# Performance work log

Hardware: AMD Instinct MI355X
Metric: run time of the kernel (lower is better)

Reference implementation:

```python
import jax, jax.numpy as jnp
import numpy as np

EPS = 1e-12
NUM_ITERATIONS = 3


def squash(t, axis=-1):
    sn = jnp.sum(t * t, axis=axis, keepdims=True)
    scale = sn / (1.0 + sn + EPS)
    return scale * t / jnp.sqrt(sn + EPS)


def setup_inputs() -> dict:
    key = jax.random.key(0)
    k1, k2 = jax.random.split(key)
    B, R, IN, OUT, C = 128, 4096, 16, 32, 2
    x = jax.random.normal(k1, (B, R, IN), dtype=jnp.float32)
    # learned parameter: torch.randn(num_capsules, num_route_nodes, in, out)
    route_weights = jax.random.normal(k2, (C, R, IN, OUT), dtype=jnp.float32)
    return {"x": x, "route_weights": route_weights}


def reference(x, route_weights):
    # priors: [C, B, R, 1, O] == x[None,:,:,None,:] @ W[:,None,:,:,:]
    priors = jnp.einsum('bri,crio->cbro', x, route_weights)[..., None, :]
    # logits kept [C,B,R,1,1]: the torch code stores [C,B,R,1,O] but every
    # update (delta_logits) is constant along O, so softmax over axis=2 is identical.
    logits = jnp.zeros(priors.shape[:-1] + (1,), dtype=priors.dtype)
    outputs = None
    for i in range(NUM_ITERATIONS):
        probs = jax.nn.softmax(logits, axis=2)                      # over route nodes
        s = jnp.sum(probs * priors, axis=2, keepdims=True)          # [C,B,1,1,O]
        outputs = squash(s, axis=-1)
        if i != NUM_ITERATIONS - 1:
            delta = jnp.sum(priors * outputs, axis=-1, keepdims=True)  # [C,B,R,1,1]
            logits = logits + delta
    return outputs
```

## Files before the change

### kernel.cpp

```cpp
#include <hip/hip_runtime.h>
#include <math.h>

#define CB    128
#define CR    4096
#define CIN   16
#define COUT  32
#define CCAP  2
#define RC    16
#define NRCH  (CR / RC)
#define EPSF  1e-12f

typedef _Float16 h8  __attribute__((ext_vector_type(8)));
typedef _Float16 h4t __attribute__((ext_vector_type(4)));
typedef float    f4  __attribute__((ext_vector_type(4)));

__global__ __launch_bounds__(256) void caps_init_kernel(float* __restrict__ vsum)
{
  vsum[blockIdx.x * 256 + threadIdx.x] = 0.f;
}

__global__ __launch_bounds__(256) void caps_prepack_kernel(
    const float* __restrict__ w, _Float16* __restrict__ wp)
{
  const int blk = (int)blockIdx.x;
  const int c   = blk >> 10;
  const int r0  = (blk & 1023) * 4;
  const int t   = (int)threadIdx.x;

  __shared__ __align__(16) float Wl[4 * 512];
  {
    const float4* src = (const float4*)(w + ((size_t)c * CR + r0) * 512);
    ((float4*)Wl)[t]       = src[t];
    ((float4*)Wl)[t + 256] = src[t + 256];
  }
  __syncthreads();

#pragma unroll
  for (int s = 0; s < 2; ++s) {
    const int idx = t + s * 256;
    const int rr  = idx >> 7;
    const int rem = idx & 127;
    const int ot  = rem >> 6;
    const int L   = rem & 63;
    const int g   = L >> 4, m = L & 15;
    h4t v;
#pragma unroll
    for (int j = 0; j < 4; ++j)
      v[j] = (_Float16)Wl[rr * 512 + (4 * g + j) * 32 + ot * 16 + m];
    *(h4t*)(wp + ((((size_t)(c * CR + r0 + rr)) * 2 + ot) * 64 + L) * 4) = v;
  }
}

__global__ __launch_bounds__(512) void caps_pass_kernel(
    const float* __restrict__ x, const _Float16* __restrict__ wp,
    const float* __restrict__ vsum,
    float* __restrict__ partialA, float* __restrict__ partialE)
{
  const int blk = (int)blockIdx.x;
  const int c   = blk >> 8;
  const int rch = blk & 255;
  const int r0  = rch * RC;
  const int t   = (int)threadIdx.x;
  const int wv  = t >> 6;
  const int L   = t & 63;
  const int g   = L >> 4;
  const int m   = L & 15;
  const int b   = wv * 16 + m;

  __shared__ __align__(16) _Float16 WpL[RC * 512];
  __shared__ float OutL[128][40];

  {
    const int4* src = (const int4*)(wp + (size_t)(c * CR + r0) * 512);
    ((int4*)WpL)[t]       = src[t];
    ((int4*)WpL)[t + 512] = src[t + 512];
  }

  const float* vb = vsum + ((size_t)c * CB + b) * COUT;
  float4 vA = *(const float4*)(vb + 4 * g);
  float4 vB = *(const float4*)(vb + 16 + 4 * g);

  float accA[4] = {0.f, 0.f, 0.f, 0.f};
  float accB[4] = {0.f, 0.f, 0.f, 0.f};
  float esum = 0.f;

  __syncthreads();

#pragma unroll 4
  for (int ri = 0; ri < RC; ++ri) {
    const int r = r0 + ri;
    float4 xf = *(const float4*)(x + ((size_t)b * CR + r) * CIN + 4 * g);
    h8 bx = {(_Float16)xf.x, (_Float16)xf.y, (_Float16)xf.z, (_Float16)xf.w,
             (_Float16)0.f, (_Float16)0.f, (_Float16)0.f, (_Float16)0.f};
    h4t wA4 = *(const h4t*)(WpL + ri * 512 + L * 4);
    h4t wB4 = *(const h4t*)(WpL + ri * 512 + 256 + L * 4);
    h8 aA = {wA4[0], wA4[1], wA4[2], wA4[3],
             (_Float16)0.f, (_Float16)0.f, (_Float16)0.f, (_Float16)0.f};
    h8 aB = {wB4[0], wB4[1], wB4[2], wB4[3],
             (_Float16)0.f, (_Float16)0.f, (_Float16)0.f, (_Float16)0.f};
    f4 z = {0.f, 0.f, 0.f, 0.f};
    f4 pA = __builtin_amdgcn_mfma_f32_16x16x32_f16(aA, bx, z, 0, 0, 0);
    f4 pB = __builtin_amdgcn_mfma_f32_16x16x32_f16(aB, bx, z, 0, 0, 0);

    float d = pA[0] * vA.x + pA[1] * vA.y + pA[2] * vA.z + pA[3] * vA.w
            + pB[0] * vB.x + pB[1] * vB.y + pB[2] * vB.z + pB[3] * vB.w;
    d += __shfl_xor(d, 16);
    d += __shfl_xor(d, 32);

    const float e = __expf(d);
    esum += e;
#pragma unroll
    for (int j = 0; j < 4; ++j) { accA[j] += e * pA[j]; accB[j] += e * pB[j]; }
  }

#pragma unroll
  for (int j = 0; j < 4; ++j) {
    OutL[b][4 * g + j]      = accA[j];
    OutL[b][16 + 4 * g + j] = accB[j];
  }
  if (g == 0) OutL[b][32] = esum;
  __syncthreads();

  {
    const int bb = t >> 2, q = t & 3;
    float4 v0 = *(const float4*)&OutL[bb][q * 8];
    float4 v1 = *(const float4*)&OutL[bb][q * 8 + 4];
    float* dst = partialA + (((size_t)(c * NRCH + rch)) * CB + bb) * COUT + q * 8;
    *(float4*)dst = v0;
    *(float4*)(dst + 4) = v1;
    if (t < 128) partialE[((size_t)(c * NRCH + rch)) * CB + t] = OutL[t][32];
  }
}

__global__ __launch_bounds__(256) void caps_redv_kernel(
    const float* __restrict__ partialA, const float* __restrict__ partialE,
    float* __restrict__ vsum, float* __restrict__ out, int final_)
{
  const int cb = (int)blockIdx.x;
  const int c  = cb >> 7, b = cb & 127;
  const int t  = (int)threadIdx.x;
  const int o  = t & 31, jg = t >> 5;

  __shared__ float red[8][33];
  __shared__ float rede[8];

  float s = 0.f;
#pragma unroll 4
  for (int k = 0; k < 32; ++k) {
    const int j = jg + k * 8;
    s += partialA[(((size_t)(c * NRCH + j)) * CB + b) * COUT + o];
  }
  red[jg][o] = s;
  __syncthreads();

  if (t < 8) {
    float e = 0.f;
#pragma unroll 4
    for (int k = 0; k < 32; ++k)
      e += partialE[((size_t)(c * NRCH + t + k * 8)) * CB + b];
    rede[t] = e;
  }
  __syncthreads();

  if (t < 32) {
    float sv = red[0][t] + red[1][t] + red[2][t] + red[3][t] +
               red[4][t] + red[5][t] + red[6][t] + red[7][t];
    float es = rede[0] + rede[1] + rede[2] + rede[3] +
               rede[4] + rede[5] + rede[6] + rede[7];
    float sm = sv / es;
    float sn = sm * sm;
#pragma unroll
    for (int sh = 1; sh < 32; sh <<= 1) sn += __shfl_xor(sn, sh);
    float fac = sn / ((1.f + sn + EPSF) * sqrtf(sn + EPSF));
    float vv = sm * fac;
    if (final_) out[cb * COUT + t] = vv;
    else        vsum[cb * COUT + t] += vv;
  }
}

extern "C" void kernel_launch(void* const* d_in, const int* in_sizes, int n_in,
                              void* d_out, int out_size, void* d_ws, size_t ws_size,
                              hipStream_t stream) {
  const float* x = (const float*)d_in[0];
  const float* w = (const float*)d_in[1];
  float* out = (float*)d_out;

  char* p = (char*)d_ws;
  _Float16* wp = (_Float16*)p;
  p += (size_t)CCAP * CR * 512 * sizeof(_Float16);
  float* vsum = (float*)p;
  p += (size_t)CCAP * CB * COUT * sizeof(float);
  float* partialA = (float*)p;
  p += (size_t)CCAP * NRCH * CB * COUT * sizeof(float);
  float* partialE = (float*)p;

  caps_prepack_kernel<<<dim3(CCAP * 1024), 256, 0, stream>>>(w, wp);
  caps_init_kernel<<<dim3(32), 256, 0, stream>>>(vsum);
  for (int it = 0; it < 3; ++it) {
    caps_pass_kernel<<<dim3(CCAP * NRCH), 512, 0, stream>>>(x, wp, vsum, partialA, partialE);
    caps_redv_kernel<<<dim3(CCAP * CB), 256, 0, stream>>>(partialA, partialE, vsum, out,
                                                          it == 2 ? 1 : 0);
  }
}
```

Baseline: 75.45 us.

## Fuse weight fp16 packing into pass kernel and drop init/prepack launches

Removes the separate prepack kernel and the vsum zero-init kernel. Each pass block now loads fp32 route weights into LDS, repacks them to fp16 in the MFMA layout in registers, and writes them back into shared memory, reusing the same LDS buffer. The first iteration takes a uniform-logit path that skips the dot product, shuffles and exp, and redv writes vsum instead of accumulating. The cost is reading fp32 weights (twice the bytes) and converting them in all three passes, instead of reading a precomputed fp16 copy.

```diff
diff --git a/kernel.cpp b/kernel.cpp
--- a/kernel.cpp
+++ b/kernel.cpp
@@ -14,47 +14,11 @@
 typedef _Float16 h4t __attribute__((ext_vector_type(4)));
 typedef float    f4  __attribute__((ext_vector_type(4)));
 
-__global__ __launch_bounds__(256) void caps_init_kernel(float* __restrict__ vsum)
-{
-  vsum[blockIdx.x * 256 + threadIdx.x] = 0.f;
-}
-
-__global__ __launch_bounds__(256) void caps_prepack_kernel(
-    const float* __restrict__ w, _Float16* __restrict__ wp)
-{
-  const int blk = (int)blockIdx.x;
-  const int c   = blk >> 10;
-  const int r0  = (blk & 1023) * 4;
-  const int t   = (int)threadIdx.x;
-
-  __shared__ __align__(16) float Wl[4 * 512];
-  {
-    const float4* src = (const float4*)(w + ((size_t)c * CR + r0) * 512);
-    ((float4*)Wl)[t]       = src[t];
-    ((float4*)Wl)[t + 256] = src[t + 256];
-  }
-  __syncthreads();
-
-#pragma unroll
-  for (int s = 0; s < 2; ++s) {
-    const int idx = t + s * 256;
-    const int rr  = idx >> 7;
-    const int rem = idx & 127;
-    const int ot  = rem >> 6;
-    const int L   = rem & 63;
-    const int g   = L >> 4, m = L & 15;
-    h4t v;
-#pragma unroll
-    for (int j = 0; j < 4; ++j)
-      v[j] = (_Float16)Wl[rr * 512 + (4 * g + j) * 32 + ot * 16 + m];
-    *(h4t*)(wp + ((((size_t)(c * CR + r0 + rr)) * 2 + ot) * 64 + L) * 4) = v;
-  }
-}
-
 __global__ __launch_bounds__(512) void caps_pass_kernel(
-    const float* __restrict__ x, const _Float16* __restrict__ wp,
+    const float* __restrict__ x, const float* __restrict__ w,
     const float* __restrict__ vsum,
-    float* __restrict__ partialA, float* __restrict__ partialE)
+    float* __restrict__ partialA, float* __restrict__ partialE,
+    int uniform)
 {
   const int blk = (int)blockIdx.x;
   const int c   = blk >> 8;
@@ -67,18 +31,41 @@
   const int m   = L & 15;
   const int b   = wv * 16 + m;
 
-  __shared__ __align__(16) _Float16 WpL[RC * 512];
-  __shared__ float OutL[128][40];
+  __shared__ __align__(16) char lds[36864];
+  float*    Wst = (float*)lds;
+  _Float16* WpL = (_Float16*)lds;
+  float (*OutL)[40] = (float (*)[40])(lds + 16384);
 
   {
-    const int4* src = (const int4*)(wp + (size_t)(c * CR + r0) * 512);
-    ((int4*)WpL)[t]       = src[t];
-    ((int4*)WpL)[t + 512] = src[t + 512];
+    const float4* src = (const float4*)(w + ((size_t)c * CR + r0) * 512);
+#pragma unroll
+    for (int k = 0; k < 4; ++k) ((float4*)Wst)[t + k * 512] = src[t + k * 512];
   }
+  __syncthreads();
 
-  const float* vb = vsum + ((size_t)c * CB + b) * COUT;
-  float4 vA = *(const float4*)(vb + 4 * g);
-  float4 vB = *(const float4*)(vb + 16 + 4 * g);
+  h4t pk[4];
+#pragma unroll
+  for (int q = 0; q < 4; ++q) {
+    const int sl  = t * 4 + q;
+    const int rr  = sl >> 7;
+    const int rem = sl & 127;
+    const int ot  = rem >> 6;
+    const int Ls  = rem & 63;
+    const int gs  = Ls >> 4, ms = Ls & 15;
+#pragma unroll
+    for (int j = 0; j < 4; ++j)
+      pk[q][j] = (_Float16)Wst[rr * 512 + (4 * gs + j) * 32 + ot * 16 + ms];
+  }
+  __syncthreads();
+#pragma unroll
+  for (int q = 0; q < 4; ++q) ((h4t*)WpL)[t * 4 + q] = pk[q];
+
+  float4 vA = {0.f, 0.f, 0.f, 0.f}, vB = {0.f, 0.f, 0.f, 0.f};
+  if (!uniform) {
+    const float* vb = vsum + ((size_t)c * CB + b) * COUT;
+    vA = *(const float4*)(vb + 4 * g);
+    vB = *(const float4*)(vb + 16 + 4 * g);
+  }
 
   float accA[4] = {0.f, 0.f, 0.f, 0.f};
   float accB[4] = {0.f, 0.f, 0.f, 0.f};
@@ -102,12 +89,16 @@
     f4 pA = __builtin_amdgcn_mfma_f32_16x16x32_f16(aA, bx, z, 0, 0, 0);
     f4 pB = __builtin_amdgcn_mfma_f32_16x16x32_f16(aB, bx, z, 0, 0, 0);
 
-    float d = pA[0] * vA.x + pA[1] * vA.y + pA[2] * vA.z + pA[3] * vA.w
-            + pB[0] * vB.x + pB[1] * vB.y + pB[2] * vB.z + pB[3] * vB.w;
-    d += __shfl_xor(d, 16);
-    d += __shfl_xor(d, 32);
-
-    const float e = __expf(d);
+    float e;
+    if (uniform) {
+      e = 1.f;
+    } else {
+      float d = pA[0] * vA.x + pA[1] * vA.y + pA[2] * vA.z + pA[3] * vA.w
+              + pB[0] * vB.x + pB[1] * vB.y + pB[2] * vB.z + pB[3] * vB.w;
+      d += __shfl_xor(d, 16);
+      d += __shfl_xor(d, 32);
+      e = __expf(d);
+    }
     esum += e;
 #pragma unroll
     for (int j = 0; j < 4; ++j) { accA[j] += e * pA[j]; accB[j] += e * pB[j]; }
@@ -134,7 +125,7 @@
 
 __global__ __launch_bounds__(256) void caps_redv_kernel(
     const float* __restrict__ partialA, const float* __restrict__ partialE,
-    float* __restrict__ vsum, float* __restrict__ out, int final_)
+    float* __restrict__ vsum, float* __restrict__ out, int mode)
 {
   const int cb = (int)blockIdx.x;
   const int c  = cb >> 7, b = cb & 127;
@@ -173,8 +164,9 @@
     for (int sh = 1; sh < 32; sh <<= 1) sn += __shfl_xor(sn, sh);
     float fac = sn / ((1.f + sn + EPSF) * sqrtf(sn + EPSF));
     float vv = sm * fac;
-    if (final_) out[cb * COUT + t] = vv;
-    else        vsum[cb * COUT + t] += vv;
+    if (mode == 2)      out[cb * COUT + t]  = vv;
+    else if (mode == 1) vsum[cb * COUT + t] += vv;
+    else                vsum[cb * COUT + t] = vv;
   }
 }
 
@@ -186,19 +178,16 @@
   float* out = (float*)d_out;
 
   char* p = (char*)d_ws;
-  _Float16* wp = (_Float16*)p;
-  p += (size_t)CCAP * CR * 512 * sizeof(_Float16);
   float* vsum = (float*)p;
   p += (size_t)CCAP * CB * COUT * sizeof(float);
   float* partialA = (float*)p;
   p += (size_t)CCAP * NRCH * CB * COUT * sizeof(float);
   float* partialE = (float*)p;
 
-  caps_prepack_kernel<<<dim3(CCAP * 1024), 256, 0, stream>>>(w, wp);
-  caps_init_kernel<<<dim3(32), 256, 0, stream>>>(vsum);
   for (int it = 0; it < 3; ++it) {
-    caps_pass_kernel<<<dim3(CCAP * NRCH), 512, 0, stream>>>(x, wp, vsum, partialA, partialE);
-    caps_redv_kernel<<<dim3(CCAP * CB), 256, 0, stream>>>(partialA, partialE, vsum, out,
-                                                          it == 2 ? 1 : 0);
+    caps_pass_kernel<<<dim3(CCAP * NRCH), 512, 0, stream>>>(
+        x, w, vsum, partialA, partialE, it == 0 ? 1 : 0);
+    caps_redv_kernel<<<dim3(CCAP * CB), 256, 0, stream>>>(
+        partialA, partialE, vsum, out, it == 0 ? 0 : (it == 1 ? 1 : 2));
   }
 }
```

Result: faster. 71.65 us (-5.0%).
